# Kernel tuning notes

Measured on AMD Instinct MI355X. Metric: run time of the kernel, lower is better.

## Reference

```python
import jax, jax.numpy as jnp
import numpy as np

N, M_DIM, CTRL = 16384, 512, 1024
EPS = 1e-16

def setup_inputs() -> dict:
    key = jax.random.key(0)
    k1, k2, k3, k4, k5 = jax.random.split(key, 5)
    embeddings = jax.random.normal(k1, (1, CTRL), dtype=jnp.float32)
    w_prev = jax.random.uniform(k2, (1, N), dtype=jnp.float32)
    w_prev = w_prev / jnp.sum(w_prev, axis=1, keepdims=True)  # valid soft address
    memory = jax.random.normal(k3, (N, M_DIM), dtype=jnp.float32) * 0.05
    out_f = 3 * M_DIM + 6  # write_lengths = [M,1,1,3,1,M,M]
    W = jax.random.normal(k4, (out_f, CTRL), dtype=jnp.float32) * (1.0 / np.sqrt(CTRL))
    b = jax.random.normal(k5, (out_f,), dtype=jnp.float32) * 0.01
    return {"embeddings": embeddings, "w_prev": w_prev, "memory": memory, "W": W, "b": b}

def reference(embeddings, w_prev, memory, W, b):
    Md = memory.shape[1]
    o = (embeddings @ W.T + b).reshape(1, -1)  # [1, 3M+6]
    # column split per write_lengths [M,1,1,3,1,M,M]
    k = o[:, :Md]
    beta = jax.nn.softplus(o[:, Md:Md + 1])
    g = jax.nn.sigmoid(o[:, Md + 1:Md + 2])
    s = jax.nn.softmax(o[:, Md + 2:Md + 5], axis=1)       # 3 circular shifts
    gamma = 1.0 + jax.nn.softplus(o[:, Md + 5:Md + 6])
    e = o[:, Md + 6:2 * Md + 6]                            # erase vector [1,M]
    a = o[:, 2 * Md + 6:]                                  # add vector   [1,M]
    # content addressing: cosine similarity of k against each memory row
    mem_norm = jnp.linalg.norm(memory, axis=1)             # [N]
    k_norm = jnp.linalg.norm(k, axis=1)                    # [1]
    sim = (k @ memory.T) / (k_norm[:, None] * mem_norm[None, :] + EPS)  # [1,N]
    wc = jax.nn.softmax(beta * sim, axis=1)
    # interpolation with previous weights
    wg = g * wc + (1.0 - g) * w_prev
    # circular convolution with 3-tap shift kernel (shifts -1,0,+1)
    ws = (s[:, 0:1] * jnp.roll(wg, 1, axis=1)
          + s[:, 1:2] * wg
          + s[:, 2:3] * jnp.roll(wg, -1, axis=1))
    # sharpening
    wp = jnp.power(ws + EPS, gamma)
    w = wp / jnp.sum(wp, axis=1, keepdims=True)            # [1,N]
    # erase/add outer-product memory write
    erase = w.T @ e                                        # [N,M]
    add = w.T @ a                                          # [N,M]
    new_memory = memory * (1.0 - erase) + add
    return w, new_memory
```

## Files before the change

kernel.cpp:

```cpp
#include <hip/hip_runtime.h>
#include <math.h>

#define N 16384
#define MD 512
#define CTRLDIM 1024
#define OUTF 1542


__device__ __forceinline__ float softplus_f(float x) {
    return (x > 20.f) ? x : log1pf(expf(x));
}

__global__ void k_proj(const float* __restrict__ emb, const float* __restrict__ W,
                       const float* __restrict__ b, float* __restrict__ O) {
    int row = blockIdx.x;
    int t = threadIdx.x;
    const float4* w4 = (const float4*)(W + (size_t)row * CTRLDIM);
    const float4* e4 = (const float4*)emb;
    float4 wv = w4[t];
    float4 ev = e4[t];
    float p = wv.x * ev.x + wv.y * ev.y + wv.z * ev.z + wv.w * ev.w;
    #pragma unroll
    for (int off = 32; off; off >>= 1) p += __shfl_down(p, off, 64);
    __shared__ float s[4];
    int lane = t & 63, wid = t >> 6;
    if (lane == 0) s[wid] = p;
    __syncthreads();
    if (t == 0) O[row] = s[0] + s[1] + s[2] + s[3] + b[row];
}

__global__ void k_scal(const float* __restrict__ O, float* __restrict__ SC,
                       float* __restrict__ E, float* __restrict__ A) {
    int t = threadIdx.x;
    float kv = O[t];
    float sq = kv * kv;
    #pragma unroll
    for (int off = 32; off; off >>= 1) sq += __shfl_down(sq, off, 64);
    __shared__ float s[8];
    int lane = t & 63, wid = t >> 6;
    if (lane == 0) s[wid] = sq;
    E[t] = O[MD + 6 + t];
    A[t] = O[2 * MD + 6 + t];
    __syncthreads();
    if (t == 0) {
        float ksq = 0.f;
        #pragma unroll
        for (int i = 0; i < 8; i++) ksq += s[i];
        float knorm = sqrtf(ksq);
        float beta = softplus_f(O[MD]);
        float g = 1.f / (1.f + expf(-O[MD + 1]));
        float s0 = O[MD + 2], s1 = O[MD + 3], s2 = O[MD + 4];
        float m = fmaxf(s0, fmaxf(s1, s2));
        float e0 = expf(s0 - m), e1 = expf(s1 - m), e2 = expf(s2 - m);
        float se = e0 + e1 + e2;
        float gamma = 1.f + softplus_f(O[MD + 5]);
        SC[0] = beta; SC[1] = g; SC[2] = e0 / se; SC[3] = e1 / se; SC[4] = e2 / se;
        SC[5] = gamma; SC[6] = knorm;
    }
}

__global__ void k_sim(const float* __restrict__ mem, const float* __restrict__ O,
                      const float* __restrict__ SC, float* __restrict__ Z) {
    int wid = threadIdx.x >> 6;
    int lane = threadIdx.x & 63;
    int row = blockIdx.x * 4 + wid;
    const float4* m4 = (const float4*)(mem + (size_t)row * MD);
    const float4* k4 = (const float4*)O;
    float dot = 0.f, nsq = 0.f;
    #pragma unroll
    for (int c = 0; c < 2; c++) {
        int j = lane + c * 64;
        float4 m = m4[j];
        float4 k = k4[j];
        dot += m.x * k.x + m.y * k.y + m.z * k.z + m.w * k.w;
        nsq += m.x * m.x + m.y * m.y + m.z * m.z + m.w * m.w;
    }
    #pragma unroll
    for (int off = 32; off; off >>= 1) {
        dot += __shfl_down(dot, off, 64);
        nsq += __shfl_down(nsq, off, 64);
    }
    if (lane == 0) {
        float beta = SC[0], knorm = SC[6];
        Z[row] = beta * dot / (knorm * sqrtf(nsq) + 1e-16f);
    }
}

__global__ void __launch_bounds__(1024) k_soft(const float* __restrict__ Z,
                                               const float* __restrict__ wprev,
                                               const float* __restrict__ SC,
                                               float* __restrict__ wout) {
    __shared__ float red[1024];
    __shared__ float sfirst[1024];
    __shared__ float slast[1024];
    int t = threadIdx.x;
    const int C = 16;
    int base = t * C;
    float z[C];
    float mx = -1e30f;
    #pragma unroll
    for (int j = 0; j < C; j++) { z[j] = Z[base + j]; mx = fmaxf(mx, z[j]); }
    red[t] = mx; __syncthreads();
    #pragma unroll
    for (int off = 512; off; off >>= 1) {
        if (t < off) red[t] = fmaxf(red[t], red[t + off]);
        __syncthreads();
    }
    mx = red[0]; __syncthreads();
    float sum = 0.f;
    #pragma unroll
    for (int j = 0; j < C; j++) { z[j] = expf(z[j] - mx); sum += z[j]; }
    red[t] = sum; __syncthreads();
    #pragma unroll
    for (int off = 512; off; off >>= 1) {
        if (t < off) red[t] += red[t + off];
        __syncthreads();
    }
    float inv = 1.f / red[0]; __syncthreads();
    float g = SC[1], s0 = SC[2], s1 = SC[3], s2 = SC[4], gamma = SC[5];
    #pragma unroll
    for (int j = 0; j < C; j++) {
        float wc = z[j] * inv;
        z[j] = g * wc + (1.f - g) * wprev[base + j];
    }
    sfirst[t] = z[0];
    slast[t] = z[C - 1];
    __syncthreads();
    float wp[C];
    float sum2 = 0.f;
    #pragma unroll
    for (int j = 0; j < C; j++) {
        float left  = (j == 0)     ? slast[(t + 1023) & 1023] : z[j - 1];
        float right = (j == C - 1) ? sfirst[(t + 1) & 1023]   : z[j + 1];
        float wsv = s0 * left + s1 * z[j] + s2 * right;
        float p = powf(wsv + 1e-16f, gamma);
        wp[j] = p;
        sum2 += p;
    }
    red[t] = sum2; __syncthreads();
    #pragma unroll
    for (int off = 512; off; off >>= 1) {
        if (t < off) red[t] += red[t + off];
        __syncthreads();
    }
    float invt = 1.f / red[0];
    #pragma unroll
    for (int j = 0; j < C; j++) wout[base + j] = wp[j] * invt;
}

__global__ void k_upd(const float* __restrict__ mem, const float* __restrict__ w,
                      const float* __restrict__ E, const float* __restrict__ A,
                      float* __restrict__ outMem) {
    int idx = blockIdx.x * blockDim.x + threadIdx.x;
    int i = idx >> 7;
    int c = idx & 127;
    float wi = w[i];
    float4 m = ((const float4*)mem)[idx];
    float4 e = ((const float4*)E)[c];
    float4 a = ((const float4*)A)[c];
    float4 o;
    o.x = m.x * (1.f - wi * e.x) + wi * a.x;
    o.y = m.y * (1.f - wi * e.y) + wi * a.y;
    o.z = m.z * (1.f - wi * e.z) + wi * a.z;
    o.w = m.w * (1.f - wi * e.w) + wi * a.w;
    ((float4*)outMem)[idx] = o;
}

extern "C" void kernel_launch(void* const* d_in, const int* in_sizes, int n_in,
                              void* d_out, int out_size, void* d_ws, size_t ws_size,
                              hipStream_t stream) {
    const float* emb   = (const float*)d_in[0];
    const float* wprev = (const float*)d_in[1];
    const float* mem   = (const float*)d_in[2];
    const float* W     = (const float*)d_in[3];
    const float* b     = (const float*)d_in[4];
    float* out = (float*)d_out;
    float* wsf = (float*)d_ws;
    float* O  = wsf;
    float* SC = wsf + 2048;
    float* E  = wsf + 2112;
    float* A  = wsf + 2688;
    float* Z  = wsf + 4096;

    k_proj<<<OUTF, 256, 0, stream>>>(emb, W, b, O);
    k_scal<<<1, 512, 0, stream>>>(O, SC, E, A);
    k_sim<<<N / 4, 256, 0, stream>>>(mem, O, SC, Z);
    k_soft<<<1, 1024, 0, stream>>>(Z, wprev, SC, out);
    k_upd<<<(N * (MD / 4)) / 256, 256, 0, stream>>>(mem, out, E, A, out + N);
}
```

Baseline: 134.9 us.

## Replace single-block softmax/sharpen kernel with fixed-shift exp and atomic global sums

The single-block softmax and sharpening kernel is split so the work is spread across the grid. The similarity kernel now computes exp(z - beta), using the fact that |cos| <= 1 so beta is an upper bound on z. Each block atomically adds its share of the softmax denominator. A new 64-block kernel does the gated interpolation, 3-tap circular shift and power sharpening, and atomically accumulates the normalizer; the update kernel then normalizes w on the fly and writes it out. This removes a 1024-thread serial reduction kernel, at the cost of atomics, order-dependent float summation and a possible underflow risk when beta is large.

```diff
diff --git a/kernel.cpp b/kernel.cpp
--- a/kernel.cpp
+++ b/kernel.cpp
@@ -30,7 +30,8 @@
 }
 
 __global__ void k_scal(const float* __restrict__ O, float* __restrict__ SC,
-                       float* __restrict__ E, float* __restrict__ A) {
+                       float* __restrict__ E, float* __restrict__ A,
+                       float* __restrict__ SUMS) {
     int t = threadIdx.x;
     float kv = O[t];
     float sq = kv * kv;
@@ -56,11 +57,14 @@
         float gamma = 1.f + softplus_f(O[MD + 5]);
         SC[0] = beta; SC[1] = g; SC[2] = e0 / se; SC[3] = e1 / se; SC[4] = e2 / se;
         SC[5] = gamma; SC[6] = knorm;
+        SUMS[0] = 0.f;
+        SUMS[1] = 0.f;
     }
 }
 
 __global__ void k_sim(const float* __restrict__ mem, const float* __restrict__ O,
-                      const float* __restrict__ SC, float* __restrict__ Z) {
+                      const float* __restrict__ SC, float* __restrict__ EZ,
+                      float* __restrict__ SUMS) {
     int wid = threadIdx.x >> 6;
     int lane = threadIdx.x & 63;
     int row = blockIdx.x * 4 + wid;
@@ -80,81 +84,54 @@
         dot += __shfl_down(dot, off, 64);
         nsq += __shfl_down(nsq, off, 64);
     }
+    __shared__ float sblk[4];
     if (lane == 0) {
         float beta = SC[0], knorm = SC[6];
-        Z[row] = beta * dot / (knorm * sqrtf(nsq) + 1e-16f);
+        float z = beta * dot / (knorm * sqrtf(nsq) + 1e-16f);
+        float ez = expf(z - beta);
+        EZ[row] = ez;
+        sblk[wid] = ez;
     }
+    __syncthreads();
+    if (threadIdx.x == 0)
+        atomicAdd(&SUMS[0], sblk[0] + sblk[1] + sblk[2] + sblk[3]);
 }
 
-__global__ void __launch_bounds__(1024) k_soft(const float* __restrict__ Z,
-                                               const float* __restrict__ wprev,
-                                               const float* __restrict__ SC,
-                                               float* __restrict__ wout) {
-    __shared__ float red[1024];
-    __shared__ float sfirst[1024];
-    __shared__ float slast[1024];
-    int t = threadIdx.x;
-    const int C = 16;
-    int base = t * C;
-    float z[C];
-    float mx = -1e30f;
+__global__ void k_shift(const float* __restrict__ EZ, const float* __restrict__ wprev,
+                        const float* __restrict__ SC, const float* __restrict__ SUMS,
+                        float* __restrict__ WP, float* __restrict__ SUMS_out) {
+    int i = blockIdx.x * 256 + threadIdx.x;
+    float inv1 = 1.f / SUMS[0];
+    float g = SC[1], s0 = SC[2], s1 = SC[3], s2 = SC[4], gamma = SC[5];
+    float gm1 = 1.f - g;
+    int im = (i == 0) ? (N - 1) : (i - 1);
+    int ip = (i == N - 1) ? 0 : (i + 1);
+    float wgm = g * EZ[im] * inv1 + gm1 * wprev[im];
+    float wgc = g * EZ[i]  * inv1 + gm1 * wprev[i];
+    float wgp = g * EZ[ip] * inv1 + gm1 * wprev[ip];
+    float wsv = s0 * wgm + s1 * wgc + s2 * wgp;
+    float wp = exp2f(gamma * log2f(wsv + 1e-16f));
+    WP[i] = wp;
     #pragma unroll
-    for (int j = 0; j < C; j++) { z[j] = Z[base + j]; mx = fmaxf(mx, z[j]); }
-    red[t] = mx; __syncthreads();
-    #pragma unroll
-    for (int off = 512; off; off >>= 1) {
-        if (t < off) red[t] = fmaxf(red[t], red[t + off]);
-        __syncthreads();
-    }
-    mx = red[0]; __syncthreads();
-    float sum = 0.f;
-    #pragma unroll
-    for (int j = 0; j < C; j++) { z[j] = expf(z[j] - mx); sum += z[j]; }
-    red[t] = sum; __syncthreads();
-    #pragma unroll
-    for (int off = 512; off; off >>= 1) {
-        if (t < off) red[t] += red[t + off];
-        __syncthreads();
-    }
-    float inv = 1.f / red[0]; __syncthreads();
-    float g = SC[1], s0 = SC[2], s1 = SC[3], s2 = SC[4], gamma = SC[5];
-    #pragma unroll
-    for (int j = 0; j < C; j++) {
-        float wc = z[j] * inv;
-        z[j] = g * wc + (1.f - g) * wprev[base + j];
-    }
-    sfirst[t] = z[0];
-    slast[t] = z[C - 1];
+    for (int off = 32; off; off >>= 1) wp += __shfl_down(wp, off, 64);
+    __shared__ float s[4];
+    int lane = threadIdx.x & 63, wid = threadIdx.x >> 6;
+    if (lane == 0) s[wid] = wp;
     __syncthreads();
-    float wp[C];
-    float sum2 = 0.f;
-    #pragma unroll
-    for (int j = 0; j < C; j++) {
-        float left  = (j == 0)     ? slast[(t + 1023) & 1023] : z[j - 1];
-        float right = (j == C - 1) ? sfirst[(t + 1) & 1023]   : z[j + 1];
-        float wsv = s0 * left + s1 * z[j] + s2 * right;
-        float p = powf(wsv + 1e-16f, gamma);
-        wp[j] = p;
-        sum2 += p;
-    }
-    red[t] = sum2; __syncthreads();
-    #pragma unroll
-    for (int off = 512; off; off >>= 1) {
-        if (t < off) red[t] += red[t + off];
-        __syncthreads();
-    }
-    float invt = 1.f / red[0];
-    #pragma unroll
-    for (int j = 0; j < C; j++) wout[base + j] = wp[j] * invt;
+    if (threadIdx.x == 0)
+        atomicAdd(&SUMS_out[1], s[0] + s[1] + s[2] + s[3]);
 }
 
-__global__ void k_upd(const float* __restrict__ mem, const float* __restrict__ w,
+__global__ void k_upd(const float* __restrict__ mem, const float* __restrict__ WP,
+                      const float* __restrict__ SUMS,
                       const float* __restrict__ E, const float* __restrict__ A,
-                      float* __restrict__ outMem) {
+                      float* __restrict__ wout, float* __restrict__ outMem) {
     int idx = blockIdx.x * blockDim.x + threadIdx.x;
     int i = idx >> 7;
     int c = idx & 127;
-    float wi = w[i];
+    float inv2 = 1.f / SUMS[1];
+    float wi = WP[i] * inv2;
+    if (c == 0) wout[i] = wi;
     float4 m = ((const float4*)mem)[idx];
     float4 e = ((const float4*)E)[c];
     float4 a = ((const float4*)A)[c];
@@ -176,15 +153,17 @@
     const float* b     = (const float*)d_in[4];
     float* out = (float*)d_out;
     float* wsf = (float*)d_ws;
-    float* O  = wsf;
-    float* SC = wsf + 2048;
-    float* E  = wsf + 2112;
-    float* A  = wsf + 2688;
-    float* Z  = wsf + 4096;
+    float* O    = wsf;
+    float* SC   = wsf + 2048;
+    float* E    = wsf + 2112;
+    float* A    = wsf + 2688;
+    float* SUMS = wsf + 3200;
+    float* EZ   = wsf + 4096;
+    float* WP   = wsf + 20480;
 
     k_proj<<<OUTF, 256, 0, stream>>>(emb, W, b, O);
-    k_scal<<<1, 512, 0, stream>>>(O, SC, E, A);
-    k_sim<<<N / 4, 256, 0, stream>>>(mem, O, SC, Z);
-    k_soft<<<1, 1024, 0, stream>>>(Z, wprev, SC, out);
-    k_upd<<<(N * (MD / 4)) / 256, 256, 0, stream>>>(mem, out, E, A, out + N);
+    k_scal<<<1, 512, 0, stream>>>(O, SC, E, A, SUMS);
+    k_sim<<<N / 4, 256, 0, stream>>>(mem, O, SC, EZ, SUMS);
+    k_shift<<<N / 256, 256, 0, stream>>>(EZ, wprev, SC, SUMS, WP, SUMS);
+    k_upd<<<(N * (MD / 4)) / 256, 256, 0, stream>>>(mem, WP, SUMS, E, A, out, out + N);
 }
```

Result: slower. 160.2 us (+18.7%).
